# Performance work log

Hardware: AMD Instinct MI355X
Metric: run time of the kernel (lower is better)

## Reference

```python
import jax, jax.numpy as jnp
import numpy as np

# init_kwargs (closed over, matching BaseDepthVolumeModel.__init__)
DEPTH_START = 0.5
DEPTH_END = 10.0
DEPTH_NUM = 64

N_SAMPLES, N_VIEWS, HEIGHT, WIDTH = 2, 4, 256, 320


def _make_extrinsics(key, shape):
    """Random small-rotation-about-y + translation world->camera 4x4 matrices."""
    ang = jax.random.uniform(key, shape, minval=-0.2, maxval=0.2)
    c, s = jnp.cos(ang), jnp.sin(ang)
    z, o = jnp.zeros_like(ang), jnp.ones_like(ang)
    R = jnp.stack([c, z, s, z, o, z, -s, z, c], axis=-1).reshape(*shape, 3, 3)
    t = jax.random.uniform(jax.random.fold_in(key, 1), (*shape, 3), minval=-0.5, maxval=0.5)
    E = jnp.zeros((*shape, 4, 4), jnp.float32)
    E = E.at[..., :3, :3].set(R).at[..., :3, 3].set(t).at[..., 3, 3].set(1.0)
    return E.astype(jnp.float32)


def setup_inputs() -> dict:
    key = jax.random.key(0)
    k1, k2 = jax.random.split(key)
    fx = fy = 200.0
    K = jnp.array([[fx, 0.0, WIDTH / 2.0], [0.0, fy, HEIGHT / 2.0], [0.0, 0.0, 1.0]], jnp.float32)
    return {
        "dst_intrinsics": jnp.broadcast_to(K, (N_SAMPLES, 1, 3, 3)),
        "dst_extrinsics": _make_extrinsics(k1, (N_SAMPLES, 1)),
        "src_intrinsics": jnp.broadcast_to(K, (N_SAMPLES, N_VIEWS, 3, 3)),
        "src_extrinsics": _make_extrinsics(k2, (N_SAMPLES, N_VIEWS)),
        "n_samples": N_SAMPLES,
        "n_views": N_VIEWS,
        "height": HEIGHT,
        "width": WIDTH,
    }


def reference(dst_intrinsics, dst_extrinsics, src_intrinsics, src_extrinsics,
              n_samples, n_views, height, width):
    # Plane-sweep target->source projection for every (sample, view, depth, pixel),
    # fully batched instead of the original triple Python loop.
    depths = jnp.linspace(DEPTH_START, DEPTH_END, DEPTH_NUM).astype(jnp.float32)  # [D]

    Kd = dst_intrinsics[:, 0]                       # [N,3,3]
    Ed = dst_extrinsics[:, 0]                       # [N,4,4]
    # relative transform source_cam <- target_cam:  T = E_src @ inv(E_dst)
    T = jnp.einsum('nvij,njk->nvik', src_extrinsics, jnp.linalg.inv(Ed))  # [N,V,4,4]
    R, t = T[..., :3, :3], T[..., :3, 3]
    A = jnp.einsum('nvij,nvjk->nvik', src_intrinsics, R)                  # K_src @ R  [N,V,3,3]
    b = jnp.einsum('nvij,nvj->nvi', src_intrinsics, t)                    # K_src @ t  [N,V,3]

    # homogeneous pixel grid of the target view, [H,W,3]
    xs = jnp.arange(width, dtype=jnp.float32)
    ys = jnp.arange(height, dtype=jnp.float32)
    X, Y = jnp.meshgrid(xs, ys, indexing='xy')
    grid_h = jnp.stack([X, Y, jnp.ones_like(X)], axis=-1)                 # [H,W,3]

    rays = jnp.einsum('nij,hwj->nhwi', jnp.linalg.inv(Kd), grid_h)        # K_dst^-1 p  [N,H,W,3]
    base = jnp.einsum('nvij,nhwj->nvhwi', A, rays)                        # [N,V,H,W,3]
    # proj = d * (K_src R K_dst^-1 p) + K_src t  -> [N,V,D,H,W,3]
    proj = depths[None, None, :, None, None, None] * base[:, :, None] + b[:, :, None, None, None, :]

    z = proj[..., 2:3]
    z_safe = jnp.where(jnp.abs(z) < 1e-8, 1e-8, z)
    xy = proj[..., :2] / z_safe                                           # source pixel coords

    in_x = (xy[..., 0:1] >= 0.0) & (xy[..., 0:1] <= width - 1)
    in_y = (xy[..., 1:2] >= 0.0) & (xy[..., 1:2] <= height - 1)
    mask = (in_x & in_y & (z > 0.0)).astype(jnp.float32)                  # [N,V,D,H,W,1]

    return xy, mask
```

## Files before the change

### kernel.cpp

```cpp
#include <hip/hip_runtime.h>
#include <math.h>

#define N_S 2
#define N_V 4
#define DQ  64
#define HH  256
#define WW  320
#define DPT 16

#define WS_IK_OFF (N_S * N_V * 12)

__global__ void setup_kernel(const float* __restrict__ Kd,
                             const float* __restrict__ Ed,
                             const float* __restrict__ Ks,
                             const float* __restrict__ Es,
                             float* __restrict__ ws) {
    int i = threadIdx.x;
    if (i >= N_S * N_V) return;
    int n = i / N_V;
    int v = i % N_V;

    const float* E = Ed + n * 16;
    float Ri[3][3], ti[3];
    for (int r = 0; r < 3; ++r)
        for (int c = 0; c < 3; ++c)
            Ri[r][c] = E[c * 4 + r];
    for (int r = 0; r < 3; ++r)
        ti[r] = -(Ri[r][0] * E[3] + Ri[r][1] * E[7] + Ri[r][2] * E[11]);

    const float* S = Es + (n * N_V + v) * 16;
    float Tr[3][3], Tt[3];
    for (int r = 0; r < 3; ++r) {
        for (int c = 0; c < 3; ++c)
            Tr[r][c] = S[r*4+0]*Ri[0][c] + S[r*4+1]*Ri[1][c] + S[r*4+2]*Ri[2][c];
        Tt[r] = S[r*4+0]*ti[0] + S[r*4+1]*ti[1] + S[r*4+2]*ti[2] + S[r*4+3];
    }

    const float* Kv = Ks + (n * N_V + v) * 9;
    float* dst = ws + i * 12;
    for (int r = 0; r < 3; ++r) {
        for (int c = 0; c < 3; ++c)
            dst[r*3+c] = Kv[r*3+0]*Tr[0][c] + Kv[r*3+1]*Tr[1][c] + Kv[r*3+2]*Tr[2][c];
        dst[9+r] = Kv[r*3+0]*Tt[0] + Kv[r*3+1]*Tt[1] + Kv[r*3+2]*Tt[2];
    }

    if (v == 0) {
        const float* Km = Kd + n * 9;
        float a=Km[0],b=Km[1],c=Km[2],d=Km[3],e=Km[4],f=Km[5],g=Km[6],h=Km[7],k=Km[8];
        float det = a*(e*k - f*h) - b*(d*k - f*g) + c*(d*h - e*g);
        float inv = 1.0f / det;
        float* ik = ws + WS_IK_OFF + n * 9;
        ik[0] =  (e*k - f*h) * inv;
        ik[1] = -(b*k - c*h) * inv;
        ik[2] =  (b*f - c*e) * inv;
        ik[3] = -(d*k - f*g) * inv;
        ik[4] =  (a*k - c*g) * inv;
        ik[5] = -(a*f - c*d) * inv;
        ik[6] =  (d*h - e*g) * inv;
        ik[7] = -(a*h - b*g) * inv;
        ik[8] =  (a*e - b*d) * inv;
    }
}

__global__ __launch_bounds__(256) void warp_kernel(const float* __restrict__ ws,
                                                   float* __restrict__ out) {
    const int HW = HH * WW;
    long long idx = (long long)blockIdx.x * blockDim.x + threadIdx.x;
    const long long total = (long long)N_S * N_V * (DQ / DPT) * HW;
    if (idx >= total) return;

    int w  = (int)(idx % WW);
    int h  = (int)((idx / WW) % HH);
    int dc = (int)((idx / HW) % (DQ / DPT));
    int nv = (int)(idx / ((long long)HW * (DQ / DPT)));
    int n  = nv / N_V;

    const float* ab = ws + nv * 12;
    float A00=ab[0],A01=ab[1],A02=ab[2];
    float A10=ab[3],A11=ab[4],A12=ab[5];
    float A20=ab[6],A21=ab[7],A22=ab[8];
    float b0=ab[9], b1=ab[10], b2=ab[11];
    const float* ik = ws + WS_IK_OFF + n * 9;

    float X = (float)w, Y = (float)h;
    float rx = ik[0]*X + ik[1]*Y + ik[2];
    float ry = ik[3]*X + ik[4]*Y + ik[5];
    float rz = ik[6]*X + ik[7]*Y + ik[8];

    float bx = A00*rx + A01*ry + A02*rz;
    float by = A10*rx + A11*ry + A12*rz;
    float bz = A20*rx + A21*ry + A22*rz;

    size_t pix    = (size_t)h * WW + w;
    size_t xybase = ((size_t)nv * DQ + (size_t)dc * DPT) * HW + pix;
    float2* __restrict__ xyout = (float2*)out;
    float*  __restrict__ mout  = out + (size_t)N_S * N_V * DQ * HW * 2;

    const float step = (float)(9.5 / 63.0);
    int d0 = dc * DPT;
    #pragma unroll
    for (int j = 0; j < DPT; ++j) {
        float depth = 0.5f + (float)(d0 + j) * step;
        float px = depth * bx + b0;
        float py = depth * by + b1;
        float pz = depth * bz + b2;
        float zs = (fabsf(pz) < 1e-8f) ? 1e-8f : pz;
        float x = px / zs;
        float y = py / zs;
        float m = (x >= 0.0f && x <= (float)(WW - 1) &&
                   y >= 0.0f && y <= (float)(HH - 1) &&
                   pz > 0.0f) ? 1.0f : 0.0f;
        size_t o = xybase + (size_t)j * HW;
        xyout[o] = make_float2(x, y);
        mout[o]  = m;
    }
}

extern "C" void kernel_launch(void* const* d_in, const int* in_sizes, int n_in,
                              void* d_out, int out_size, void* d_ws, size_t ws_size,
                              hipStream_t stream) {
    const float* Kd = (const float*)d_in[0];
    const float* Ed = (const float*)d_in[1];
    const float* Ks = (const float*)d_in[2];
    const float* Es = (const float*)d_in[3];
    float* ws = (float*)d_ws;

    hipLaunchKernelGGL(setup_kernel, dim3(1), dim3(64), 0, stream, Kd, Ed, Ks, Es, ws);

    long long total = (long long)N_S * N_V * (DQ / DPT) * HH * WW;
    int blocks = (int)((total + 255) / 256);
    hipLaunchKernelGGL(warp_kernel, dim3(blocks), dim3(256), 0, stream,
                       (const float*)ws, (float*)d_out);
}
```

Before: 103.7 us.

## Fuse setup into warp kernel, process two pixels per thread with nontemporal stores

Removes the separate single-block setup kernel by having each thread recompute the relative transform and the inverse intrinsics from the inputs. Each thread now handles two adjacent pixels, which widens stores to 16-byte xy and 8-byte mask vectors, and those stores are nontemporal. This saves one launch and a dependency, at the cost of redundant per-thread matrix math and extra input loads. The output is write-bound (about 126 MB), so the wider and nontemporal stores are aimed at write efficiency.

```diff
diff --git a/kernel.cpp b/kernel.cpp
--- a/kernel.cpp
+++ b/kernel.cpp
@@ -6,113 +6,133 @@
 #define DQ  64
 #define HH  256
 #define WW  320
+#define WW2 (WW / 2)
 #define DPT 16
+#define NDC (DQ / DPT)
 
-#define WS_IK_OFF (N_S * N_V * 12)
+typedef float f32x4 __attribute__((ext_vector_type(4)));
+typedef float f32x2 __attribute__((ext_vector_type(2)));
 
-__global__ void setup_kernel(const float* __restrict__ Kd,
-                             const float* __restrict__ Ed,
-                             const float* __restrict__ Ks,
-                             const float* __restrict__ Es,
-                             float* __restrict__ ws) {
-    int i = threadIdx.x;
-    if (i >= N_S * N_V) return;
-    int n = i / N_V;
-    int v = i % N_V;
+__global__ __launch_bounds__(256) void fused_warp_kernel(
+    const float* __restrict__ Kd,
+    const float* __restrict__ Ed,
+    const float* __restrict__ Ks,
+    const float* __restrict__ Es,
+    float* __restrict__ out)
+{
+    const int HW = HH * WW;
+    int idx = blockIdx.x * 256 + threadIdx.x;
+
+    int w2 = idx % WW2;
+    int tt = idx / WW2;
+    int h  = tt % HH;
+    tt /= HH;
+    int dc = tt % NDC;
+    int nv = tt / NDC;
+    int n  = nv >> 2;
 
     const float* E = Ed + n * 16;
     float Ri[3][3], ti[3];
+    #pragma unroll
     for (int r = 0; r < 3; ++r)
+        #pragma unroll
         for (int c = 0; c < 3; ++c)
             Ri[r][c] = E[c * 4 + r];
+    #pragma unroll
     for (int r = 0; r < 3; ++r)
         ti[r] = -(Ri[r][0] * E[3] + Ri[r][1] * E[7] + Ri[r][2] * E[11]);
 
-    const float* S = Es + (n * N_V + v) * 16;
+    const float* S = Es + nv * 16;
     float Tr[3][3], Tt[3];
+    #pragma unroll
     for (int r = 0; r < 3; ++r) {
+        #pragma unroll
         for (int c = 0; c < 3; ++c)
             Tr[r][c] = S[r*4+0]*Ri[0][c] + S[r*4+1]*Ri[1][c] + S[r*4+2]*Ri[2][c];
         Tt[r] = S[r*4+0]*ti[0] + S[r*4+1]*ti[1] + S[r*4+2]*ti[2] + S[r*4+3];
     }
 
-    const float* Kv = Ks + (n * N_V + v) * 9;
-    float* dst = ws + i * 12;
-    for (int r = 0; r < 3; ++r) {
-        for (int c = 0; c < 3; ++c)
-            dst[r*3+c] = Kv[r*3+0]*Tr[0][c] + Kv[r*3+1]*Tr[1][c] + Kv[r*3+2]*Tr[2][c];
-        dst[9+r] = Kv[r*3+0]*Tt[0] + Kv[r*3+1]*Tt[1] + Kv[r*3+2]*Tt[2];
+    const float* Kv = Ks + nv * 9;
+    float A00,A01,A02,A10,A11,A12,A20,A21,A22,b0,b1,b2;
+    {
+        float Am[3][3], bm[3];
+        #pragma unroll
+        for (int r = 0; r < 3; ++r) {
+            #pragma unroll
+            for (int c = 0; c < 3; ++c)
+                Am[r][c] = Kv[r*3+0]*Tr[0][c] + Kv[r*3+1]*Tr[1][c] + Kv[r*3+2]*Tr[2][c];
+            bm[r] = Kv[r*3+0]*Tt[0] + Kv[r*3+1]*Tt[1] + Kv[r*3+2]*Tt[2];
+        }
+        A00=Am[0][0];A01=Am[0][1];A02=Am[0][2];
+        A10=Am[1][0];A11=Am[1][1];A12=Am[1][2];
+        A20=Am[2][0];A21=Am[2][1];A22=Am[2][2];
+        b0=bm[0];b1=bm[1];b2=bm[2];
     }
 
-    if (v == 0) {
+    float ik0,ik1,ik2,ik3,ik4,ik5,ik6,ik7,ik8;
+    {
         const float* Km = Kd + n * 9;
-        float a=Km[0],b=Km[1],c=Km[2],d=Km[3],e=Km[4],f=Km[5],g=Km[6],h=Km[7],k=Km[8];
-        float det = a*(e*k - f*h) - b*(d*k - f*g) + c*(d*h - e*g);
+        float a=Km[0],b=Km[1],c=Km[2],d=Km[3],e=Km[4],f=Km[5],g=Km[6],hh=Km[7],k=Km[8];
+        float det = a*(e*k - f*hh) - b*(d*k - f*g) + c*(d*hh - e*g);
         float inv = 1.0f / det;
-        float* ik = ws + WS_IK_OFF + n * 9;
-        ik[0] =  (e*k - f*h) * inv;
-        ik[1] = -(b*k - c*h) * inv;
-        ik[2] =  (b*f - c*e) * inv;
-        ik[3] = -(d*k - f*g) * inv;
-        ik[4] =  (a*k - c*g) * inv;
-        ik[5] = -(a*f - c*d) * inv;
-        ik[6] =  (d*h - e*g) * inv;
-        ik[7] = -(a*h - b*g) * inv;
-        ik[8] =  (a*e - b*d) * inv;
+        ik0 =  (e*k - f*hh) * inv;
+        ik1 = -(b*k - c*hh) * inv;
+        ik2 =  (b*f - c*e) * inv;
+        ik3 = -(d*k - f*g) * inv;
+        ik4 =  (a*k - c*g) * inv;
+        ik5 = -(a*f - c*d) * inv;
+        ik6 =  (d*hh - e*g) * inv;
+        ik7 = -(a*hh - b*g) * inv;
+        ik8 =  (a*e - b*d) * inv;
     }
-}
 
-__global__ __launch_bounds__(256) void warp_kernel(const float* __restrict__ ws,
-                                                   float* __restrict__ out) {
-    const int HW = HH * WW;
-    long long idx = (long long)blockIdx.x * blockDim.x + threadIdx.x;
-    const long long total = (long long)N_S * N_V * (DQ / DPT) * HW;
-    if (idx >= total) return;
+    float X0 = (float)(2 * w2), X1 = X0 + 1.0f, Y = (float)h;
 
-    int w  = (int)(idx % WW);
-    int h  = (int)((idx / WW) % HH);
-    int dc = (int)((idx / HW) % (DQ / DPT));
-    int nv = (int)(idx / ((long long)HW * (DQ / DPT)));
-    int n  = nv / N_V;
+    float rx0 = ik0*X0 + ik1*Y + ik2;
+    float ry0 = ik3*X0 + ik4*Y + ik5;
+    float rz0 = ik6*X0 + ik7*Y + ik8;
+    float rx1 = ik0*X1 + ik1*Y + ik2;
+    float ry1 = ik3*X1 + ik4*Y + ik5;
+    float rz1 = ik6*X1 + ik7*Y + ik8;
 
-    const float* ab = ws + nv * 12;
-    float A00=ab[0],A01=ab[1],A02=ab[2];
-    float A10=ab[3],A11=ab[4],A12=ab[5];
-    float A20=ab[6],A21=ab[7],A22=ab[8];
-    float b0=ab[9], b1=ab[10], b2=ab[11];
-    const float* ik = ws + WS_IK_OFF + n * 9;
+    float bx0 = A00*rx0 + A01*ry0 + A02*rz0;
+    float by0 = A10*rx0 + A11*ry0 + A12*rz0;
+    float bz0 = A20*rx0 + A21*ry0 + A22*rz0;
+    float bx1 = A00*rx1 + A01*ry1 + A02*rz1;
+    float by1 = A10*rx1 + A11*ry1 + A12*rz1;
+    float bz1 = A20*rx1 + A21*ry1 + A22*rz1;
 
-    float X = (float)w, Y = (float)h;
-    float rx = ik[0]*X + ik[1]*Y + ik[2];
-    float ry = ik[3]*X + ik[4]*Y + ik[5];
-    float rz = ik[6]*X + ik[7]*Y + ik[8];
-
-    float bx = A00*rx + A01*ry + A02*rz;
-    float by = A10*rx + A11*ry + A12*rz;
-    float bz = A20*rx + A21*ry + A22*rz;
-
-    size_t pix    = (size_t)h * WW + w;
-    size_t xybase = ((size_t)nv * DQ + (size_t)dc * DPT) * HW + pix;
-    float2* __restrict__ xyout = (float2*)out;
-    float*  __restrict__ mout  = out + (size_t)N_S * N_V * DQ * HW * 2;
+    size_t pixbase = ((size_t)nv * DQ + (size_t)dc * DPT) * HW
+                   + (size_t)h * WW + (size_t)(2 * w2);
+    float* __restrict__ mout = out + (size_t)N_S * N_V * DQ * HW * 2;
 
     const float step = (float)(9.5 / 63.0);
     int d0 = dc * DPT;
+
     #pragma unroll
     for (int j = 0; j < DPT; ++j) {
         float depth = 0.5f + (float)(d0 + j) * step;
-        float px = depth * bx + b0;
-        float py = depth * by + b1;
-        float pz = depth * bz + b2;
-        float zs = (fabsf(pz) < 1e-8f) ? 1e-8f : pz;
-        float x = px / zs;
-        float y = py / zs;
-        float m = (x >= 0.0f && x <= (float)(WW - 1) &&
-                   y >= 0.0f && y <= (float)(HH - 1) &&
-                   pz > 0.0f) ? 1.0f : 0.0f;
-        size_t o = xybase + (size_t)j * HW;
-        xyout[o] = make_float2(x, y);
-        mout[o]  = m;
+
+        float px0 = depth*bx0 + b0, py0 = depth*by0 + b1, pz0 = depth*bz0 + b2;
+        float px1 = depth*bx1 + b0, py1 = depth*by1 + b1, pz1 = depth*bz1 + b2;
+
+        float zs0 = (fabsf(pz0) < 1e-8f) ? 1e-8f : pz0;
+        float zs1 = (fabsf(pz1) < 1e-8f) ? 1e-8f : pz1;
+
+        float x0 = px0 / zs0, y0 = py0 / zs0;
+        float x1 = px1 / zs1, y1 = py1 / zs1;
+
+        float m0 = (x0 >= 0.0f && x0 <= (float)(WW-1) &&
+                    y0 >= 0.0f && y0 <= (float)(HH-1) && pz0 > 0.0f) ? 1.0f : 0.0f;
+        float m1 = (x1 >= 0.0f && x1 <= (float)(WW-1) &&
+                    y1 >= 0.0f && y1 <= (float)(HH-1) && pz1 > 0.0f) ? 1.0f : 0.0f;
+
+        size_t p = pixbase + (size_t)j * HW;
+
+        f32x4 xyv; xyv.x = x0; xyv.y = y0; xyv.z = x1; xyv.w = y1;
+        __builtin_nontemporal_store(xyv, (f32x4*)(out + 2 * p));
+        f32x2 mv; mv.x = m0; mv.y = m1;
+        __builtin_nontemporal_store(mv, (f32x2*)(mout + p));
     }
 }
 
@@ -123,12 +143,9 @@
     const float* Ed = (const float*)d_in[1];
     const float* Ks = (const float*)d_in[2];
     const float* Es = (const float*)d_in[3];
-    float* ws = (float*)d_ws;
 
-    hipLaunchKernelGGL(setup_kernel, dim3(1), dim3(64), 0, stream, Kd, Ed, Ks, Es, ws);
-
-    long long total = (long long)N_S * N_V * (DQ / DPT) * HH * WW;
+    const long long total = (long long)N_S * N_V * NDC * HH * WW2;
     int blocks = (int)((total + 255) / 256);
-    hipLaunchKernelGGL(warp_kernel, dim3(blocks), dim3(256), 0, stream,
-                       (const float*)ws, (float*)d_out);
+    hipLaunchKernelGGL(fused_warp_kernel, dim3(blocks), dim3(256), 0, stream,
+                       Kd, Ed, Ks, Es, (float*)d_out);
 }
```

After: 94.95 us. 8.4% less time.
